# Kernel tuning notes

Measured on AMD Instinct MI355X. Metric: run time of the kernel, lower is better.

Reference implementation:

```python
import jax, jax.numpy as jnp
import numpy as np

N = 768
SINGLE_DIM = 384
PAIR_DIM = 128
D = 16      # proj_dim per head
H = 12      # n_heads
P = 4       # n_query_points
PV = 8      # n_point_values


def _random_rotations(key, n):
    a = jax.random.normal(key, (n, 3, 3), dtype=jnp.float32)
    q, r = jnp.linalg.qr(a)
    d = jnp.sign(jnp.diagonal(r, axis1=-2, axis2=-1))
    q = q * d[:, None, :]
    det = jnp.linalg.det(q)
    return q * jnp.where(det < 0, -1.0, 1.0)[:, None, None]


def setup_inputs() -> dict:
    key = jax.random.key(0)
    ks = jax.random.split(key, 12)
    s = 0.02
    return {
        "single_rep": jax.random.normal(ks[0], (N, SINGLE_DIM), dtype=jnp.float32),
        "pair_rep": jax.random.normal(ks[1], (N, N, PAIR_DIM), dtype=jnp.float32),
        "rotations": _random_rotations(ks[2], N),
        "translations": jax.random.normal(ks[3], (N, 3), dtype=jnp.float32),
        "Wqkv": s * jax.random.normal(ks[4], (SINGLE_DIM, 3 * H * D), dtype=jnp.float32),
        "Wb": s * jax.random.normal(ks[5], (PAIR_DIM, H), dtype=jnp.float32),
        "Wqk_pts": s * jax.random.normal(ks[6], (SINGLE_DIM, 2 * H * P * 3), dtype=jnp.float32),
        "Wv_pts": s * jax.random.normal(ks[7], (SINGLE_DIM, H * PV * 3), dtype=jnp.float32),
        "gamma": 0.1 * jax.random.normal(ks[8], (H,), dtype=jnp.float32),
        "Wout": s * jax.random.normal(ks[9], (H * (PAIR_DIM + D + PV * 3 + PV), SINGLE_DIM), dtype=jnp.float32),
        "bout": jnp.zeros((SINGLE_DIM,), dtype=jnp.float32),
    }


def _apply_frames(rot, trans, pts):
    # pts: [N, P, H, 3] -> R @ pt + t per residue (dim 0)
    return jnp.einsum('nba,npha->nphb', rot, pts) + trans[:, None, None, :]


def _apply_frames_inv(rot, trans, pts):
    # R^T (pt - t)
    return jnp.einsum('nab,npha->nphb', rot, pts - trans[:, None, None, :])


def reference(single_rep, pair_rep, rotations, translations,
              Wqkv, Wb, Wqk_pts, Wv_pts, gamma, Wout, bout):
    n = single_rep.shape[0]
    sqrt_inv_dim = 1.0 / np.sqrt(D).astype(np.float32)
    w_C = np.sqrt(2.0 / (9.0 * P)).astype(np.float32)
    w_L = np.sqrt(1.0 / 3.0).astype(np.float32)

    qkv = single_rep @ Wqkv                       # [N, 3*H*D]
    q, k, v = jnp.split(qkv, 3, axis=-1)
    q = q.reshape(n, D, H)
    k = k.reshape(n, D, H)
    v = v.reshape(n, D, H)

    b = pair_rep @ Wb                             # [N, N, H]

    qk_pts = single_rep @ Wqk_pts
    q_pts, k_pts = jnp.split(qk_pts, 2, axis=-1)
    q_pts = jnp.moveaxis(q_pts.reshape(n, P, 3, H), -1, -2)   # [N, P, H, 3]
    k_pts = jnp.moveaxis(k_pts.reshape(n, P, 3, H), -1, -2)
    v_pts = jnp.moveaxis((single_rep @ Wv_pts).reshape(n, PV, 3, H), -1, -2)  # [N, PV, H, 3]

    qg = _apply_frames(rotations, translations, q_pts)  # [N, P, H, 3]
    kg = _apply_frames(rotations, translations, k_pts)

    # sum_{p,t} ||qg_i - kg_j||^2 via expansion (avoids [N,N,P,H,3])
    q_sq = jnp.sum(qg * qg, axis=(1, 3))                # [N, H]
    k_sq = jnp.sum(kg * kg, axis=(1, 3))                # [N, H]
    cross = jnp.einsum('ipht,jpht->ijh', qg, kg)        # [N, N, H]
    dist_logits = q_sq[:, None, :] + k_sq[None, :, :] - 2.0 * cross

    dp_logits = sqrt_inv_dim * jnp.einsum('idh,jdh->ijh', q, k) + b
    scale = gamma * (w_C / 2.0)                          # [H]
    a = jax.nn.softmax(w_L * (dp_logits - scale * dist_logits), axis=1)  # [N, N, H]

    out_pair = jnp.einsum('ijh,ijz->izh', a, pair_rep)   # [N, pair_dim, H]
    out_value = jnp.einsum('ijh,jdh->idh', a, v)          # [N, D, H]

    vg = _apply_frames(rotations, translations, v_pts)    # [N, PV, H, 3]
    op = jnp.einsum('ijh,jpht->ipht', a, vg)              # [N, PV, H, 3]
    out_points = _apply_frames_inv(rotations, translations, op)
    out_points_norm = jnp.linalg.norm(out_points, axis=-1)  # [N, PV, H]

    out = jnp.concatenate([
        out_pair.reshape(n, -1),
        out_value.reshape(n, -1),
        out_points.reshape(n, -1),
        out_points_norm.reshape(n, -1),
    ], axis=1)
    return out @ Wout + bout
```

## Files before the change

### kernel.cpp

```cpp
#include <hip/hip_runtime.h>
#include <math.h>

#define NN 768
#define SD 384
#define HH 12

#define W_L 0.57735026918962576f
#define W_C 0.23570226039551584f

typedef __attribute__((ext_vector_type(8))) short short8;
typedef __attribute__((ext_vector_type(4))) float floatx4;
typedef unsigned short ushort_t;
typedef unsigned int uint_t;

__device__ __forceinline__ float wave_max(float v){ for(int o=32;o;o>>=1) v=fmaxf(v,__shfl_xor(v,o)); return v; }
__device__ __forceinline__ float wave_sum(float v){ for(int o=32;o;o>>=1) v+=__shfl_xor(v,o); return v; }

static __device__ __forceinline__ ushort_t f2bf(float f) {
  union { float f; uint_t u; } v; v.f = f;
  uint_t r = (v.u + 0x7FFFu + ((v.u >> 16) & 1u)) >> 16;
  return (ushort_t)r;
}
static __device__ __forceinline__ uint_t pack2bf(float lo, float hi) {
  return ((uint_t)f2bf(hi) << 16) | (uint_t)f2bf(lo);
}

__global__ __launch_bounds__(256) void k1a_gemm(
    const float* __restrict__ single, const float* __restrict__ Wqkv,
    const float* __restrict__ Wqk, const float* __restrict__ Wvp,
    float* __restrict__ raw)
{
  __shared__ float Al[64][17];
  __shared__ float Bl[16][68];
  const int tid = threadIdx.x;
  const int bm = blockIdx.x / 18, bn = blockIdx.x % 18;
  const int tr = tid >> 4, tc = tid & 15;

  const int bcol = bn*64 + (tid & 15)*4;
  const float* Wsrc; int wstride;
  if (bcol < 576)      { Wsrc = Wqkv + bcol;        wstride = 576; }
  else if (bcol < 864) { Wsrc = Wqk  + (bcol-576);  wstride = 288; }
  else                 { Wsrc = Wvp  + (bcol-864);  wstride = 288; }
  const int brow = tid >> 4;
  const int ar = tid >> 2, ac = (tid & 3)*4;

  float4 acc0 = {0,0,0,0}, acc1 = {0,0,0,0}, acc2 = {0,0,0,0}, acc3 = {0,0,0,0};

  for (int kc = 0; kc < 24; ++kc) {
    __syncthreads();
    *(float4*)&Al[ar][ac] = *(const float4*)(single + (size_t)(bm*64+ar)*SD + kc*16 + ac);
    *(float4*)&Bl[brow][(tid&15)*4] = *(const float4*)(Wsrc + (size_t)(kc*16+brow)*wstride);
    __syncthreads();
    #pragma unroll
    for (int kk = 0; kk < 16; ++kk) {
      float a0 = Al[tr*4+0][kk], a1 = Al[tr*4+1][kk], a2 = Al[tr*4+2][kk], a3 = Al[tr*4+3][kk];
      float4 bv = *(float4*)&Bl[kk][tc*4];
      acc0.x += a0*bv.x; acc0.y += a0*bv.y; acc0.z += a0*bv.z; acc0.w += a0*bv.w;
      acc1.x += a1*bv.x; acc1.y += a1*bv.y; acc1.z += a1*bv.z; acc1.w += a1*bv.w;
      acc2.x += a2*bv.x; acc2.y += a2*bv.y; acc2.z += a2*bv.z; acc2.w += a2*bv.w;
      acc3.x += a3*bv.x; acc3.y += a3*bv.y; acc3.z += a3*bv.z; acc3.w += a3*bv.w;
    }
  }
  float* o = raw + (size_t)(bm*64 + tr*4)*1152 + bn*64 + tc*4;
  *(float4*)(o)            = acc0;
  *(float4*)(o + 1152)     = acc1;
  *(float4*)(o + 2*1152)   = acc2;
  *(float4*)(o + 3*1152)   = acc3;
}

__global__ __launch_bounds__(256) void k1b_pack(
    const float* __restrict__ raw_g, const float* __restrict__ rot,
    const float* __restrict__ trans, const float* __restrict__ gamma,
    float* __restrict__ Qt, ushort_t* __restrict__ Ktb, ushort_t* __restrict__ vvT)
{
  __shared__ float raw[4][1152];
  __shared__ float gbuf[4][16][HH][3];
  const int tid = threadIdx.x;
  const int i0 = blockIdx.x * 4;

  for (int s = tid; s < 4*288; s += 256) {
    int r = s / 288, q = s % 288;
    *(float4*)(&raw[r][q*4]) = *(const float4*)(raw_g + (size_t)(i0+r)*1152 + q*4);
  }
  __syncthreads();

  for (int s = tid; s < 4*576; s += 256) {
    int r = s / 576, cc = s % 576;
    int d = (cc % 192) / HH, h = cc % HH;
    int i = i0 + r;
    float val = raw[r][cc];
    if (cc < 192)       Qt[(size_t)i*384 + h*32 + d] = 0.25f*W_L*val;
    else if (cc < 384)  Ktb[(size_t)i*384 + h*32 + d] = f2bf(val);
    else                vvT[(size_t)(h*40 + d)*768 + i] = f2bf(val);
  }
  for (int s = tid; s < 768; s += 256) {
    int r = s / 192, rem = s % 192;
    int slot = rem / HH, h = rem % HH;
    int i = i0 + r;
    int base;
    if (slot < 4) base = 576 + slot*36;
    else if (slot < 8) base = 720 + (slot-4)*36;
    else base = 864 + (slot-8)*36;
    float x0 = raw[r][base + 0*12 + h];
    float x1 = raw[r][base + 1*12 + h];
    float x2 = raw[r][base + 2*12 + h];
    const float* R = rot + (size_t)i*9;
    const float* T = trans + (size_t)i*3;
    float g0 = R[0]*x0 + R[1]*x1 + R[2]*x2 + T[0];
    float g1 = R[3]*x0 + R[4]*x1 + R[5]*x2 + T[1];
    float g2 = R[6]*x0 + R[7]*x1 + R[8]*x2 + T[2];
    gbuf[r][slot][h][0]=g0; gbuf[r][slot][h][1]=g1; gbuf[r][slot][h][2]=g2;
    if (slot < 4) {
      float sc2 = 2.0f*W_L*(gamma[h]*W_C*0.5f);
      float* q = Qt + (size_t)i*384 + h*32 + 16 + slot*3;
      q[0]=sc2*g0; q[1]=sc2*g1; q[2]=sc2*g2;
    } else if (slot < 8) {
      ushort_t* k = Ktb + (size_t)i*384 + h*32 + 16 + (slot-4)*3;
      k[0]=f2bf(g0); k[1]=f2bf(g1); k[2]=f2bf(g2);
    } else {
      ushort_t* vp = vvT + (size_t)(h*40 + 16 + (slot-8)*3)*768 + i;
      vp[0]=f2bf(g0); vp[768]=f2bf(g1); vp[2*768]=f2bf(g2);
    }
  }
  __syncthreads();
  for (int s = tid; s < 96; s += 256) {
    int r = s / 24, rem = s % 24;
    int h = rem / 2, qk = rem % 2;
    int i = i0 + r;
    float sum = 0;
    int b0 = qk ? 4 : 0;
    for (int p = 0; p < 4; ++p)
      for (int t = 0; t < 3; ++t) { float g = gbuf[r][b0+p][h][t]; sum += g*g; }
    float sc = gamma[h]*W_C*0.5f;
    if (qk == 0) {
      float* q = Qt + (size_t)i*384 + h*32;
      q[28] = -W_L*sc; q[29] = -W_L*sc*sum; q[30] = 0.f; q[31] = 0.f;
    } else {
      ushort_t* k = Ktb + (size_t)i*384 + h*32;
      k[28] = f2bf(sum); k[29] = f2bf(1.f); k[30] = 0; k[31] = 0;
    }
  }
}

__global__ __launch_bounds__(256) void k2t_logits(
    const float* __restrict__ pair, const float* __restrict__ Wb,
    const float* __restrict__ Qt, const ushort_t* __restrict__ Ktb,
    float* __restrict__ L, ushort_t* __restrict__ Tzg)
{
  __shared__ ushort_t Tj[64*136];
  __shared__ ushort_t WbT[16*136];
  __shared__ float Qrow[384];
  const int tid = threadIdx.x;
  const int i = blockIdx.x / 12;
  const int j0 = (blockIdx.x % 12) * 64;
  const int lane = tid & 63;
  const int w = tid >> 6;
  const int co = lane & 15, gg = lane >> 4;

  for (int s = tid; s < 1536; s += 256) {
    int z = s / 12, h = s % 12;
    WbT[h*136 + z] = f2bf(W_L * Wb[s]);
  }
  for (int s = tid; s < 544; s += 256) WbT[1632 + s] = 0;
  for (int s = tid; s < 384; s += 256) Qrow[s] = Qt[(size_t)i*384 + s];

  const float* src = pair + ((size_t)i*NN + j0)*128;
  float4 pv[8];
  #pragma unroll
  for (int k = 0; k < 8; ++k) {
    int f = tid + k*256;
    int row = f >> 5, zq = f & 31;
    pv[k] = *(const float4*)(src + (size_t)row*128 + zq*4);
  }
  #pragma unroll
  for (int k = 0; k < 8; ++k) {
    int f = tid + k*256;
    int row = f >> 5, zq = f & 31;
    uint_t* d = (uint_t*)&Tj[row*136 + zq*4];
    d[0] = pack2bf(pv[k].x, pv[k].y);
    d[1] = pack2bf(pv[k].z, pv[k].w);
  }
  __syncthreads();

  short8 z8, myQ, wb[4];
  #pragma unroll
  for (int s = 0; s < 8; ++s) z8[s] = 0;
  #pragma unroll
  for (int s = 0; s < 8; ++s)
    myQ[s] = (co < 12) ? (short)f2bf(Qrow[co*32 + gg*8 + s]) : (short)0;
  #pragma unroll
  for (int kt = 0; kt < 4; ++kt)
    wb[kt] = *(const short8*)&WbT[co*136 + kt*32 + gg*8];

  const int jb = w*16;
  floatx4 D; D[0]=0.f; D[1]=0.f; D[2]=0.f; D[3]=0.f;
  #pragma unroll
  for (int kt = 0; kt < 4; ++kt) {
    short8 a = *(const short8*)&Tj[(jb+co)*136 + kt*32 + gg*8];
    D = __builtin_amdgcn_mfma_f32_16x16x32_bf16(a, wb[kt], D, 0, 0, 0);
  }
  const ushort_t* kr = Ktb + (size_t)(j0 + jb + co)*384;
  #pragma unroll
  for (int kt = 0; kt < 12; ++kt) {
    short8 a = *(const short8*)(kr + kt*32 + gg*8);
    short8 b = (co == kt) ? myQ : z8;
    D = __builtin_amdgcn_mfma_f32_16x16x32_bf16(a, b, D, 0, 0, 0);
  }
  if (co < 12) {
    float4 st = {D[0], D[1], D[2], D[3]};
    *(float4*)(L + ((size_t)i*12 + co)*768 + j0 + jb + gg*4) = st;
  }

  const int z = tid & 127, jg = tid >> 7;
  uint_t ow[16];
  #pragma unroll
  for (int m = 0; m < 16; ++m) {
    ushort_t a = Tj[(jg*32 + 2*m)*136 + z];
    ushort_t b = Tj[(jg*32 + 2*m + 1)*136 + z];
    ow[m] = ((uint_t)b << 16) | (uint_t)a;
  }
  ushort_t* dst = Tzg + ((size_t)i*128 + z)*768 + j0 + jg*32;
  #pragma unroll
  for (int q = 0; q < 4; ++q) {
    uint4 u4 = {ow[q*4+0], ow[q*4+1], ow[q*4+2], ow[q*4+3]};
    *(uint4*)(dst + q*8) = u4;
  }
}

__global__ __launch_bounds__(512) void k3g(
    const float* __restrict__ L, const ushort_t* __restrict__ Tzg,
    const ushort_t* __restrict__ vvT, const float* __restrict__ rot,
    const float* __restrict__ trans, float* __restrict__ C2)
{
  __shared__ ushort_t PTb[24*512];
  __shared__ float oacc[480];
  const int tid = threadIdx.x;
  const int i = (NN - 1) - blockIdx.x;
  const int w = tid >> 6, lane = tid & 63;
  const int co = lane & 15, gg = lane >> 4;

  const float* Lr = L + (size_t)i*12*768;
  #pragma unroll
  for (int m = 0; m < 2; ++m) {
    if (m == 1 && w >= 4) break;
    const int h = (m == 0) ? w : 8 + w;
    const float* row = Lr + (size_t)h*768;
    float mx = -1e30f;
    #pragma unroll
    for (int k = 0; k < 12; ++k) mx = fmaxf(mx, row[lane + 64*k]);
    mx = wave_max(mx);
    float ev[12]; float sm = 0.f;
    #pragma unroll
    for (int k = 0; k < 12; ++k) { ev[k] = __expf(row[lane + 64*k] - mx); sm += ev[k]; }
    sm = wave_sum(sm);
    const float inv = 1.0f / sm;
    #pragma unroll
    for (int k = 0; k < 12; ++k) {
      int jj = lane + 64*k;
      PTb[(jj >> 5)*512 + h*32 + (jj & 31)] = f2bf(ev[k]*inv);
    }
  }
  for (int s = tid; s < 3072; s += 512) {
    int t = s >> 7, rest = s & 127;
    PTb[t*512 + 384 + rest] = 0;
  }
  __syncthreads();

  floatx4 accZ; accZ[0]=0.f; accZ[1]=0.f; accZ[2]=0.f; accZ[3]=0.f;
  floatx4 accV[4];
  #pragma unroll
  for (int u = 0; u < 4; ++u) { accV[u][0]=0.f; accV[u][1]=0.f; accV[u][2]=0.f; accV[u][3]=0.f; }

  const bool full = (w*4 + 2 < 30);
  const ushort_t* tz  = Tzg + ((size_t)i*128 + w*16 + co)*768 + gg*8;
  const ushort_t* vb0 = vvT + (size_t)((w*4+0)*16 + co)*768 + gg*8;
  const ushort_t* vb1 = vvT + (size_t)((w*4+1)*16 + co)*768 + gg*8;
  const ushort_t* vb2 = vvT + (size_t)((w*4+2)*16 + co)*768 + gg*8;
  const ushort_t* vb3 = vvT + (size_t)((w*4+3)*16 + co)*768 + gg*8;

  short8 nT  = *(const short8*)(tz);
  short8 nV0 = *(const short8*)(vb0);
  short8 nV1 = *(const short8*)(vb1);
  short8 nV2 = nT, nV3 = nT;
  if (full) { nV2 = *(const short8*)(vb2); nV3 = *(const short8*)(vb3); }

  #pragma unroll 1
  for (int t = 0; t < 24; ++t) {
    short8 cT = nT, cV0 = nV0, cV1 = nV1, cV2 = nV2, cV3 = nV3;
    if (t < 23) {
      const int toff = (t+1)*32;
      nT  = *(const short8*)(tz  + toff);
      nV0 = *(const short8*)(vb0 + toff);
      nV1 = *(const short8*)(vb1 + toff);
      if (full) {
        nV2 = *(const short8*)(vb2 + toff);
        nV3 = *(const short8*)(vb3 + toff);
      }
    }
    const short8 aP = *(const short8*)&PTb[t*512 + co*32 + gg*8];
    accZ    = __builtin_amdgcn_mfma_f32_16x16x32_bf16(aP, cT,  accZ,    0, 0, 0);
    accV[0] = __builtin_amdgcn_mfma_f32_16x16x32_bf16(aP, cV0, accV[0], 0, 0, 0);
    accV[1] = __builtin_amdgcn_mfma_f32_16x16x32_bf16(aP, cV1, accV[1], 0, 0, 0);
    if (full) {
      accV[2] = __builtin_amdgcn_mfma_f32_16x16x32_bf16(aP, cV2, accV[2], 0, 0, 0);
      accV[3] = __builtin_amdgcn_mfma_f32_16x16x32_bf16(aP, cV3, accV[3], 0, 0, 0);
    }
  }

  float* o = C2 + (size_t)i*2112;
  #pragma unroll
  for (int r = 0; r < 4; ++r) {
    int h = gg*4 + r;
    if (h < 12) o[(w*16 + co)*12 + h] = accZ[r];
  }
  #pragma unroll
  for (int u = 0; u < 4; ++u) {
    int cb = w*4 + u;
    if (cb < 30) {
      int c = cb*16 + co;
      int hc = c / 40;
      #pragma unroll
      for (int r = 0; r < 4; ++r)
        if (gg*4 + r == hc) oacc[c] = accV[u][r];
    }
  }
  __syncthreads();

  if (tid < 96) {
    const int pp = tid / 12, hh = tid % 12;
    const float* R = rot + (size_t)i*9;
    const float* T = trans + (size_t)i*3;
    float x0 = oacc[hh*40+16+pp*3+0] - T[0];
    float x1 = oacc[hh*40+16+pp*3+1] - T[1];
    float x2 = oacc[hh*40+16+pp*3+2] - T[2];
    float y0 = R[0]*x0 + R[3]*x1 + R[6]*x2;
    float y1 = R[1]*x0 + R[4]*x1 + R[7]*x2;
    float y2 = R[2]*x0 + R[5]*x1 + R[8]*x2;
    o[1728 + pp*36 + hh*3 + 0] = y0;
    o[1728 + pp*36 + hh*3 + 1] = y1;
    o[1728 + pp*36 + hh*3 + 2] = y2;
    o[2016 + pp*12 + hh] = sqrtf(y0*y0 + y1*y1 + y2*y2);
  } else if (tid < 288) {
    const int c = tid - 96;
    int d = c / 12, hh = c % 12;
    o[1536 + d*12 + hh] = oacc[hh*40 + d];
  }
}

__global__ __launch_bounds__(256) void k5_out(
    const float* __restrict__ C2, const float* __restrict__ Wout,
    const float* __restrict__ bout, float* __restrict__ out)
{
  __shared__ float Al[32*68];
  __shared__ float Bl[64*36];
  const int tid = threadIdx.x;
  const int bm = blockIdx.x / 12, bn = blockIdx.x % 12;
  const int tr = tid / 16, tc = tid % 16;
  float acc00=0, acc01=0, acc10=0, acc11=0;
  for (int kc = 0; kc < 33; ++kc) {
    __syncthreads();
    for (int s = tid; s < 512; s += 256) {
      int row = s / 16, kq = s % 16;
      *(float4*)(&Al[row*68 + kq*4]) =
        *(const float4*)(C2 + (size_t)(bm*32+row)*2112 + kc*64 + kq*4);
    }
    for (int s = tid; s < 512; s += 256) {
      int kk = s / 8, cq = s % 8;
      *(float4*)(&Bl[kk*36 + cq*4]) =
        *(const float4*)(Wout + (size_t)(kc*64+kk)*384 + bn*32 + cq*4);
    }
    __syncthreads();
    for (int kk = 0; kk < 64; ++kk) {
      float a0 = Al[(tr*2)*68 + kk], a1 = Al[(tr*2+1)*68 + kk];
      float b0 = Bl[kk*36 + tc*2], b1 = Bl[kk*36 + tc*2 + 1];
      acc00 += a0*b0; acc01 += a0*b1;
      acc10 += a1*b0; acc11 += a1*b1;
    }
  }
  int r0 = bm*32 + tr*2, c0 = bn*32 + tc*2;
  out[(size_t)r0*384 + c0]       = acc00 + bout[c0];
  out[(size_t)r0*384 + c0+1]     = acc01 + bout[c0+1];
  out[(size_t)(r0+1)*384 + c0]   = acc10 + bout[c0];
  out[(size_t)(r0+1)*384 + c0+1] = acc11 + bout[c0+1];
}

extern "C" void kernel_launch(void* const* d_in, const int* in_sizes, int n_in,
                              void* d_out, int out_size, void* d_ws, size_t ws_size,
                              hipStream_t stream)
{
  const float* single = (const float*)d_in[0];
  const float* pair   = (const float*)d_in[1];
  const float* rot    = (const float*)d_in[2];
  const float* trans  = (const float*)d_in[3];
  const float* Wqkv   = (const float*)d_in[4];
  const float* Wb     = (const float*)d_in[5];
  const float* Wqk    = (const float*)d_in[6];
  const float* Wvp    = (const float*)d_in[7];
  const float* gamma  = (const float*)d_in[8];
  const float* Wout   = (const float*)d_in[9];
  const float* bout   = (const float*)d_in[10];

  float* ws   = (float*)d_ws;
  float* raw  = ws;
  float* Qt   = raw + (size_t)768*1152;
  float* C2   = Qt  + (size_t)768*384;
  float* L    = C2  + (size_t)768*2112;
  ushort_t* Ktb = (ushort_t*)(L + (size_t)768*12*768);
  ushort_t* vvT = Ktb + (size_t)768*384;
  ushort_t* Tzg = vvT + (size_t)480*768;
  float* out  = (float*)d_out;

  k1a_gemm<<<dim3(216), dim3(256), 0, stream>>>(single, Wqkv, Wqk, Wvp, raw);
  k1b_pack<<<dim3(192), dim3(256), 0, stream>>>(raw, rot, trans, gamma, Qt, Ktb, vvT);
  k2t_logits<<<dim3(9216), dim3(256), 0, stream>>>(pair, Wb, Qt, Ktb, L, Tzg);
  k3g<<<dim3(768), dim3(512), 0, stream>>>(L, Tzg, vvT, rot, trans, C2);
  k5_out<<<dim3(288), dim3(256), 0, stream>>>(C2, Wout, bout, out);
}
```

Measured before the change: 373.5 us.

## Pad LDS tiles, prefetch K fragments early, double-buffer global loads in k3g

In k2t_logits the K fragments are now loaded from global memory into registers before the pair tile is staged, so their latency overlaps the staging work. The LDS row stride is padded from 136 to 140 to reduce bank conflicts. In k3g the probability tile in LDS gets a padded per-head stride (34) and row stride (544), and the MFMA loop keeps two steps of loads in flight instead of one. Launch bounds gain occupancy hints (3 and 4 blocks). The deeper prefetch and the hoisted fragments raise register pressure, which the occupancy hints may push into spills.

```diff
diff --git a/kernel.cpp b/kernel.cpp
--- a/kernel.cpp
+++ b/kernel.cpp
@@ -142,12 +142,13 @@
   }
 }
 
-__global__ __launch_bounds__(256) void k2t_logits(
+#define TJS 140
+__global__ __launch_bounds__(256, 3) void k2t_logits(
     const float* __restrict__ pair, const float* __restrict__ Wb,
     const float* __restrict__ Qt, const ushort_t* __restrict__ Ktb,
     float* __restrict__ L, ushort_t* __restrict__ Tzg)
 {
-  __shared__ ushort_t Tj[64*136];
+  __shared__ ushort_t Tj[64*TJS];
   __shared__ ushort_t WbT[16*136];
   __shared__ float Qrow[384];
   const int tid = threadIdx.x;
@@ -156,6 +157,7 @@
   const int lane = tid & 63;
   const int w = tid >> 6;
   const int co = lane & 15, gg = lane >> 4;
+  const int jb = w*16;
 
   for (int s = tid; s < 1536; s += 256) {
     int z = s / 12, h = s % 12;
@@ -163,6 +165,14 @@
   }
   for (int s = tid; s < 544; s += 256) WbT[1632 + s] = 0;
   for (int s = tid; s < 384; s += 256) Qrow[s] = Qt[(size_t)i*384 + s];
+
+  short8 kf[12];
+  {
+    const ushort_t* kr = Ktb + (size_t)(j0 + jb + co)*384;
+    #pragma unroll
+    for (int kt = 0; kt < 12; ++kt)
+      kf[kt] = *(const short8*)(kr + kt*32 + gg*8);
+  }
 
   const float* src = pair + ((size_t)i*NN + j0)*128;
   float4 pv[8];
@@ -176,7 +186,7 @@
   for (int k = 0; k < 8; ++k) {
     int f = tid + k*256;
     int row = f >> 5, zq = f & 31;
-    uint_t* d = (uint_t*)&Tj[row*136 + zq*4];
+    uint_t* d = (uint_t*)&Tj[row*TJS + zq*4];
     d[0] = pack2bf(pv[k].x, pv[k].y);
     d[1] = pack2bf(pv[k].z, pv[k].w);
   }
@@ -192,19 +202,16 @@
   for (int kt = 0; kt < 4; ++kt)
     wb[kt] = *(const short8*)&WbT[co*136 + kt*32 + gg*8];
 
-  const int jb = w*16;
   floatx4 D; D[0]=0.f; D[1]=0.f; D[2]=0.f; D[3]=0.f;
   #pragma unroll
   for (int kt = 0; kt < 4; ++kt) {
-    short8 a = *(const short8*)&Tj[(jb+co)*136 + kt*32 + gg*8];
+    short8 a = *(const short8*)&Tj[(jb+co)*TJS + kt*32 + gg*8];
     D = __builtin_amdgcn_mfma_f32_16x16x32_bf16(a, wb[kt], D, 0, 0, 0);
   }
-  const ushort_t* kr = Ktb + (size_t)(j0 + jb + co)*384;
   #pragma unroll
   for (int kt = 0; kt < 12; ++kt) {
-    short8 a = *(const short8*)(kr + kt*32 + gg*8);
     short8 b = (co == kt) ? myQ : z8;
-    D = __builtin_amdgcn_mfma_f32_16x16x32_bf16(a, b, D, 0, 0, 0);
+    D = __builtin_amdgcn_mfma_f32_16x16x32_bf16(kf[kt], b, D, 0, 0, 0);
   }
   if (co < 12) {
     float4 st = {D[0], D[1], D[2], D[3]};
@@ -215,8 +222,8 @@
   uint_t ow[16];
   #pragma unroll
   for (int m = 0; m < 16; ++m) {
-    ushort_t a = Tj[(jg*32 + 2*m)*136 + z];
-    ushort_t b = Tj[(jg*32 + 2*m + 1)*136 + z];
+    ushort_t a = Tj[(jg*32 + 2*m)*TJS + z];
+    ushort_t b = Tj[(jg*32 + 2*m + 1)*TJS + z];
     ow[m] = ((uint_t)b << 16) | (uint_t)a;
   }
   ushort_t* dst = Tzg + ((size_t)i*128 + z)*768 + j0 + jg*32;
@@ -227,12 +234,13 @@
   }
 }
 
-__global__ __launch_bounds__(512) void k3g(
+#define PTS 544
+__global__ __launch_bounds__(512, 4) void k3g(
     const float* __restrict__ L, const ushort_t* __restrict__ Tzg,
     const ushort_t* __restrict__ vvT, const float* __restrict__ rot,
     const float* __restrict__ trans, float* __restrict__ C2)
 {
-  __shared__ ushort_t PTb[24*512];
+  __shared__ ushort_t PTb[24*PTS];
   __shared__ float oacc[480];
   const int tid = threadIdx.x;
   const int i = (NN - 1) - blockIdx.x;
@@ -257,12 +265,12 @@
     #pragma unroll
     for (int k = 0; k < 12; ++k) {
       int jj = lane + 64*k;
-      PTb[(jj >> 5)*512 + h*32 + (jj & 31)] = f2bf(ev[k]*inv);
-    }
-  }
-  for (int s = tid; s < 3072; s += 512) {
-    int t = s >> 7, rest = s & 127;
-    PTb[t*512 + 384 + rest] = 0;
+      PTb[(jj >> 5)*PTS + h*34 + (jj & 31)] = f2bf(ev[k]*inv);
+    }
+  }
+  for (int s = tid; s < 24*136; s += 512) {
+    int t = s / 136, r = s % 136;
+    PTb[t*PTS + 408 + r] = 0;
   }
   __syncthreads();
 
@@ -278,32 +286,60 @@
   const ushort_t* vb2 = vvT + (size_t)((w*4+2)*16 + co)*768 + gg*8;
   const ushort_t* vb3 = vvT + (size_t)((w*4+3)*16 + co)*768 + gg*8;
 
-  short8 nT  = *(const short8*)(tz);
-  short8 nV0 = *(const short8*)(vb0);
-  short8 nV1 = *(const short8*)(vb1);
-  short8 nV2 = nT, nV3 = nT;
-  if (full) { nV2 = *(const short8*)(vb2); nV3 = *(const short8*)(vb3); }
+  short8 aT  = *(const short8*)(tz);
+  short8 aV0 = *(const short8*)(vb0);
+  short8 aV1 = *(const short8*)(vb1);
+  short8 aV2 = aT, aV3 = aT;
+  short8 bT  = *(const short8*)(tz  + 32);
+  short8 bV0 = *(const short8*)(vb0 + 32);
+  short8 bV1 = *(const short8*)(vb1 + 32);
+  short8 bV2 = bT, bV3 = bT;
+  if (full) {
+    aV2 = *(const short8*)(vb2);      aV3 = *(const short8*)(vb3);
+    bV2 = *(const short8*)(vb2 + 32); bV3 = *(const short8*)(vb3 + 32);
+  }
 
   #pragma unroll 1
-  for (int t = 0; t < 24; ++t) {
-    short8 cT = nT, cV0 = nV0, cV1 = nV1, cV2 = nV2, cV3 = nV3;
-    if (t < 23) {
-      const int toff = (t+1)*32;
-      nT  = *(const short8*)(tz  + toff);
-      nV0 = *(const short8*)(vb0 + toff);
-      nV1 = *(const short8*)(vb1 + toff);
+  for (int tt = 0; tt < 24; tt += 2) {
+    {
+      const short8 aP = *(const short8*)&PTb[tt*PTS + co*34 + gg*8];
+      accZ    = __builtin_amdgcn_mfma_f32_16x16x32_bf16(aP, aT,  accZ,    0, 0, 0);
+      accV[0] = __builtin_amdgcn_mfma_f32_16x16x32_bf16(aP, aV0, accV[0], 0, 0, 0);
+      accV[1] = __builtin_amdgcn_mfma_f32_16x16x32_bf16(aP, aV1, accV[1], 0, 0, 0);
       if (full) {
-        nV2 = *(const short8*)(vb2 + toff);
-        nV3 = *(const short8*)(vb3 + toff);
+        accV[2] = __builtin_amdgcn_mfma_f32_16x16x32_bf16(aP, aV2, accV[2], 0, 0, 0);
+        accV[3] = __builtin_amdgcn_mfma_f32_16x16x32_bf16(aP, aV3, accV[3], 0, 0, 0);
       }
     }
-    const short8 aP = *(const short8*)&PTb[t*512 + co*32 + gg*8];
-    accZ    = __builtin_amdgcn_mfma_f32_16x16x32_bf16(aP, cT,  accZ,    0, 0, 0);
-    accV[0] = __builtin_amdgcn_mfma_f32_16x16x32_bf16(aP, cV0, accV[0], 0, 0, 0);
-    accV[1] = __builtin_amdgcn_mfma_f32_16x16x32_bf16(aP, cV1, accV[1], 0, 0, 0);
-    if (full) {
-      accV[2] = __builtin_amdgcn_mfma_f32_16x16x32_bf16(aP, cV2, accV[2], 0, 0, 0);
-      accV[3] = __builtin_amdgcn_mfma_f32_16x16x32_bf16(aP, cV3, accV[3], 0, 0, 0);
+    if (tt + 2 < 24) {
+      const int toff = (tt+2)*32;
+      aT  = *(const short8*)(tz  + toff);
+      aV0 = *(const short8*)(vb0 + toff);
+      aV1 = *(const short8*)(vb1 + toff);
+      if (full) {
+        aV2 = *(const short8*)(vb2 + toff);
+        aV3 = *(const short8*)(vb3 + toff);
+      }
+    }
+    {
+      const short8 aP = *(const short8*)&PTb[(tt+1)*PTS + co*34 + gg*8];
+      accZ    = __builtin_amdgcn_mfma_f32_16x16x32_bf16(aP, bT,  accZ,    0, 0, 0);
+      accV[0] = __builtin_amdgcn_mfma_f32_16x16x32_bf16(aP, bV0, accV[0], 0, 0, 0);
+      accV[1] = __builtin_amdgcn_mfma_f32_16x16x32_bf16(aP, bV1, accV[1], 0, 0, 0);
+      if (full) {
+        accV[2] = __builtin_amdgcn_mfma_f32_16x16x32_bf16(aP, bV2, accV[2], 0, 0, 0);
+        accV[3] = __builtin_amdgcn_mfma_f32_16x16x32_bf16(aP, bV3, accV[3], 0, 0, 0);
+      }
+    }
+    if (tt + 3 < 24) {
+      const int toff = (tt+3)*32;
+      bT  = *(const short8*)(tz  + toff);
+      bV0 = *(const short8*)(vb0 + toff);
+      bV1 = *(const short8*)(vb1 + toff);
+      if (full) {
+        bV2 = *(const short8*)(vb2 + toff);
+        bV3 = *(const short8*)(vb3 + toff);
+      }
     }
   }
 
```

New measurement: 354.0 us. 5.2% less time.
